# Optimization experiments

Hardware: AMD Instinct MI355X
Metric: run time of the kernel (lower is better)

The kernel has to match this reference:

```python
import jax, jax.numpy as jnp
import numpy as np

NL, NQ, FD, HD, NH = 6, 128, 256, 512, 8
NC, B, T, H, W = 6, 1, 1, 48, 120
PPF = 24 // 6  # points_per_face
P = PPF * PPF * 6  # code emits (num_points//6)^2 points per face = 96 total
NPARAM, NTYPE, NATTR = 11, 10, 3
PMIN = np.array([-50., -50., -5., -15., -15., -5., -5., -3.14, 0.5, 0.5, 0.5], np.float32)
PMAX = np.array([50., 50., 5., 15., 15., 5., 5., 3.14, 10., 5., 3.], np.float32)


def _box_template():
    off = np.linspace(-0.4, 0.4, PPF).astype(np.float32)
    pts = []
    for axis in range(3):  # -x,+x,-y,+y,-z,+z faces, same order as torch code
        for s in (-0.5, 0.5):
            rem = [a for a in range(3) if a != axis]
            for i in range(PPF):
                for j in range(PPF):
                    p = [0.0, 0.0, 0.0]
                    p[axis] = s
                    p[rem[0]] = off[i]
                    p[rem[1]] = off[j]
                    pts.append(p)
    return np.asarray(pts, np.float32)  # [P,3]

TPL = _box_template()


def _mlp2(x, w1, b1, w2, b2):
    return jax.nn.relu(x @ w1.T + b1) @ w2.T + b2


def _ln(x, g, b):
    m = x.mean(-1, keepdims=True)
    v = ((x - m) ** 2).mean(-1, keepdims=True)
    return (x - m) * jax.lax.rsqrt(v + 1e-5) * g + b


def _mha(q, k, v, in_w, in_b, out_w, out_b):
    hd = HD // NH
    wq, wk, wv = jnp.split(in_w, 3, axis=0)
    bq, bk, bv = jnp.split(in_b, 3)
    def heads(x, w, b):
        y = x @ w.T + b
        return y.reshape(x.shape[0], x.shape[1], NH, hd).transpose(0, 2, 1, 3)
    Q, K, V = heads(q, wq, bq), heads(k, wk, bk), heads(v, wv, bv)
    a = jax.nn.softmax(jnp.einsum('bhqd,bhkd->bhqk', Q, K) * (hd ** -0.5), axis=-1)
    o = jnp.einsum('bhqk,bhkd->bhqd', a, V)
    o = o.transpose(0, 2, 1, 3).reshape(q.shape[0], q.shape[1], HD)
    return o @ out_w.T + out_b


def _sample_box_points(motion):
    # motion [B,N,11] -> [B,N,P,3]; indices: X0 Y1 Z2 .. YAW7 L8 W9 H10
    c = motion[..., 0:3]
    dims = motion[..., 8:11]
    yaw = motion[..., 7]
    p = TPL * dims[:, :, None, :]  # [B,N,P,3]
    cy, sy = jnp.cos(yaw)[..., None], jnp.sin(yaw)[..., None]
    xr = p[..., 0] * cy - p[..., 1] * sy
    yr = p[..., 0] * sy + p[..., 1] * cy
    return jnp.stack([xr, yr, p[..., 2]], -1) + c[:, :, None, :]


def _gather_aggregate(pts, features, proj):
    # pts [B,N,P,3]; features [NC,B,T,C,H,W]; proj [NC,3,4]
    Bb, N, Pp, _ = pts.shape
    NP = N * Pp
    hom = jnp.concatenate([pts, jnp.ones_like(pts[..., :1])], -1)
    feat_flat = features.reshape(NC, Bb, T, FD, H * W)
    acc = jnp.zeros((Bb, FD, NP), features.dtype)
    for cidx in range(NC):
        cam = jnp.einsum('ij,bnpj->bnpi', proj[cidx], hom)  # [B,N,P,3]
        z = cam[..., 2]
        zs = jnp.where(jnp.abs(z) > 1e-6, z, 1e-6)
        u = (cam[..., 0] / zs).reshape(Bb, NP)
        v = (cam[..., 1] / zs).reshape(Bb, NP)
        front = (z > 0).reshape(Bb, NP)
        u0, v0 = jnp.floor(u), jnp.floor(v)
        du, dv = u - u0, v - v0
        cam_acc = jnp.zeros((Bb, T, FD, NP), features.dtype)
        for (ui, vi, wgt) in ((u0, v0, (1 - du) * (1 - dv)),
                              (u0 + 1, v0, du * (1 - dv)),
                              (u0, v0 + 1, (1 - du) * dv),
                              (u0 + 1, v0 + 1, du * dv)):
            ok = front & (ui >= 0) & (ui <= W - 1) & (vi >= 0) & (vi <= H - 1)
            idx = (jnp.clip(vi, 0, H - 1) * W + jnp.clip(ui, 0, W - 1)).astype(jnp.int32)
            bidx = jnp.broadcast_to(idx[:, None, None, :], (Bb, T, FD, NP))
            g = jnp.take_along_axis(feat_flat[cidx], bidx, axis=-1)
            cam_acc = cam_acc + g * (wgt * ok)[:, None, None, :]
        acc = acc + cam_acc.mean(axis=1)  # mean over time
    agg = (acc / NC).reshape(Bb, FD, N, Pp).mean(-1)  # mean over cams and points
    return agg.transpose(0, 2, 1)  # [B,N,C]

_ga = jax.checkpoint(_gather_aggregate)


def _forward(features, proj, ego_states, queries0, param_min, param_max, motion_w1, motion_b1, motion_w2, motion_b2, type_w1, type_b1, type_w2, type_b2, attr_w1, attr_b1, attr_w2, attr_b2, fmlp_w1, fmlp_b1, fmlp_w2, fmlp_b2, sa_in_w, sa_in_b, sa_out_w, sa_out_b, fa_in_w, fa_in_b, fa_out_w, fa_out_b, ffn_w1, ffn_b1, ffn_w2, ffn_b2, ln1_g, ln1_b, ln2_g, ln2_b, ln3_g, ln3_b):
    Bb = features.shape[1]
    q = jnp.broadcast_to(queries0, (Bb, NQ, HD))
    preds = []
    for i in range(NL):
        motion = jax.nn.sigmoid(_mlp2(q, motion_w1, motion_b1, motion_w2, motion_b2)) * (param_max - param_min) + param_min
        tlog = _mlp2(q, type_w1, type_b1, type_w2, type_b2)
        attr = jax.nn.sigmoid(_mlp2(q, attr_w1, attr_b1, attr_w2, attr_b2))
        preds.append(jnp.concatenate([motion, tlog, attr], -1))
        if i == NL - 1:
            break  # last layer only predicts (layers[-1] unused, as in torch code)
        pts = _sample_box_points(motion)
        agg = _ga(pts, features, proj)
        feat_h = _mlp2(agg, fmlp_w1, fmlp_b1, fmlp_w2, fmlp_b2)
        x = _ln(q, ln1_g[i], ln1_b[i])
        x = x + _mha(x, x, x, sa_in_w[i], sa_in_b[i], sa_out_w[i], sa_out_b[i])
        x = _ln(x, ln2_g[i], ln2_b[i])
        x = x + _mha(x, feat_h, feat_h, fa_in_w[i], fa_in_b[i], fa_out_w[i], fa_out_b[i])
        x = _ln(x, ln3_g[i], ln3_b[i])
        q = x + _mlp2(x, ffn_w1[i], ffn_b1[i], ffn_w2[i], ffn_b2[i])
    return jnp.stack(preds)  # [NL,B,NQ,24]


def setup_inputs() -> dict:
    key = jax.random.key(0)
    ks = iter(jax.random.split(key, 64))
    def g(shape, s=0.02):
        return jax.random.normal(next(ks), shape, jnp.float32) * s
    fx, cx, cy = 40.0, W / 2.0, H / 2.0
    Ps = []
    for c in range(NC):
        th = 2.0 * np.pi * c / NC
        Rm = np.stack([np.array([-np.sin(th), np.cos(th), 0.0]),
                       np.array([0.0, 0.0, -1.0]),
                       np.array([np.cos(th), np.sin(th), 0.0])])
        K = np.array([[fx, 0.0, cx], [0.0, fx, cy], [0.0, 0.0, 1.0]])
        Pm = np.zeros((3, 4))
        Pm[:, :3] = K @ Rm
        Ps.append(Pm)
    inp = dict(
        features=jax.random.normal(next(ks), (NC, B, T, FD, H, W), jnp.float32),
        proj=jnp.asarray(np.asarray(Ps, np.float32)),
        ego_states=jax.random.normal(next(ks), (B, T, 5), jnp.float32),
        queries0=g((1, NQ, HD), 1.0),
        param_min=jnp.asarray(PMIN), param_max=jnp.asarray(PMAX),
        motion_w1=g((HD, HD)), motion_b1=jnp.zeros((HD,)),
        motion_w2=g((NPARAM, HD)), motion_b2=jnp.zeros((NPARAM,)),
        type_w1=g((HD, HD)), type_b1=jnp.zeros((HD,)),
        type_w2=g((NTYPE, HD)), type_b2=jnp.zeros((NTYPE,)),
        attr_w1=g((HD, HD)), attr_b1=jnp.zeros((HD,)),
        attr_w2=g((NATTR, HD)), attr_b2=jnp.zeros((NATTR,)),
        fmlp_w1=g((HD, FD)), fmlp_b1=jnp.zeros((HD,)),
        fmlp_w2=g((HD, HD)), fmlp_b2=jnp.zeros((HD,)),
        sa_in_w=g((NL, 3 * HD, HD)), sa_in_b=jnp.zeros((NL, 3 * HD)),
        sa_out_w=g((NL, HD, HD)), sa_out_b=jnp.zeros((NL, HD)),
        fa_in_w=g((NL, 3 * HD, HD)), fa_in_b=jnp.zeros((NL, 3 * HD)),
        fa_out_w=g((NL, HD, HD)), fa_out_b=jnp.zeros((NL, HD)),
        ffn_w1=g((NL, 4 * HD, HD)), ffn_b1=jnp.zeros((NL, 4 * HD)),
        ffn_w2=g((NL, HD, 4 * HD)), ffn_b2=jnp.zeros((NL, HD)),
        ln1_g=jnp.ones((NL, HD)), ln1_b=jnp.zeros((NL, HD)),
        ln2_g=jnp.ones((NL, HD)), ln2_b=jnp.zeros((NL, HD)),
        ln3_g=jnp.ones((NL, HD)), ln3_b=jnp.zeros((NL, HD)),
    )
    return inp


def reference(features, proj, ego_states, queries0, param_min, param_max, motion_w1, motion_b1, motion_w2, motion_b2, type_w1, type_b1, type_w2, type_b2, attr_w1, attr_b1, attr_w2, attr_b2, fmlp_w1, fmlp_b1, fmlp_w2, fmlp_b2, sa_in_w, sa_in_b, sa_out_w, sa_out_b, fa_in_w, fa_in_b, fa_out_w, fa_out_b, ffn_w1, ffn_b1, ffn_w2, ffn_b2, ln1_g, ln1_b, ln2_g, ln2_b, ln3_g, ln3_b):
    return _forward(features, proj, ego_states, queries0, param_min, param_max, motion_w1, motion_b1, motion_w2, motion_b2, type_w1, type_b1, type_w2, type_b2, attr_w1, attr_b1, attr_w2, attr_b2, fmlp_w1, fmlp_b1, fmlp_w2, fmlp_b2, sa_in_w, sa_in_b, sa_out_w, sa_out_b, fa_in_w, fa_in_b, fa_out_w, fa_out_b, ffn_w1, ffn_b1, ffn_w2, ffn_b2, ln1_g, ln1_b, ln2_g, ln2_b, ln3_g, ln3_b)
```

## Files before the change

### kernel.cpp

```cpp
#include <hip/hip_runtime.h>
#include <hip/hip_bf16.h>

typedef __hip_bfloat16 bf16;
typedef _Float16 h16;
typedef __attribute__((ext_vector_type(8))) _Float16 half8;
typedef __attribute__((ext_vector_type(4))) _Float16 half4;
typedef __attribute__((ext_vector_type(4))) float f32x4;

#define NQ 128
#define HD 512
#define FD 256
#define NC 6
#define IMH 48
#define IMW 120
#define HW 5760

__device__ __forceinline__ half8 pack8(float4 x, float4 y) {
    half8 h;
    h[0] = (h16)x.x; h[1] = (h16)x.y; h[2] = (h16)x.z; h[3] = (h16)x.w;
    h[4] = (h16)y.x; h[5] = (h16)y.y; h[6] = (h16)y.z; h[7] = (h16)y.w;
    return h;
}

__global__ __launch_bounds__(256) void transpose_feat_k(const float* __restrict__ f,
                                                        bf16* __restrict__ ft)
{
    __shared__ float tile[32][33];
    int cam = blockIdx.z;
    int hw0 = blockIdx.x * 32, fd0 = blockIdx.y * 32;
    int tx = threadIdx.x, ty = threadIdx.y;
    const float* fb = f + (size_t)cam * FD * HW;
    for (int r = ty; r < 32; r += 8)
        tile[r][tx] = fb[(size_t)(fd0 + r) * HW + hw0 + tx];
    __syncthreads();
    bf16* fo = ft + (size_t)cam * HW * FD;
    for (int r = ty; r < 32; r += 8)
        fo[(size_t)(hw0 + r) * FD + fd0 + tx] = __float2bfloat16(tile[tx][r]);
}

__global__ __launch_bounds__(256) void cvt16_k(const float* __restrict__ src,
                                               h16* __restrict__ dst, int n)
{
    int i = blockIdx.x * 256 + threadIdx.x;
    if (i < n) dst[i] = (h16)src[i];
}

struct SwzDesc {
    const float* src[11];
    unsigned int chunkStart[12];
    unsigned int tileStart[11];
    int K[11];
};

__device__ __forceinline__ int lperm(int lane, int ksl) {
    return lane ^ ((lane >> 4) & 3) ^ (ksl << 2);
}

__global__ __launch_bounds__(256) void swizzle3_k(SwzDesc d, h16* __restrict__ dst)
{
    __shared__ h16 fbuf[4096];
    int bid = blockIdx.x;
    int w = 0;
    while (bid >= (int)d.chunkStart[w + 1]) w++;
    int local = bid - (int)d.chunkStart[w];
    int Kk = d.K[w];
    int kc = Kk >> 6;
    int n64 = local / kc, kchunk = local - n64 * kc;
    int t = threadIdx.x;

    int rr  = t >> 4;
    int cb  = (t & 15) * 4;
    int ksl = (t >> 3) & 1;
    int kk  = cb & 31;
    int laneb = ((kk >> 3) << 4) + rr;
    int elemB = (kk & 7) * 2;
    const float* sbase = d.src[w] + (size_t)(n64 * 64 + rr) * Kk + kchunk * 64 + cb;
#pragma unroll
    for (int rp = 0; rp < 4; rp++) {
        float4 u = *(const float4*)(sbase + (size_t)rp * 16 * Kk);
        int tile8 = ksl * 4 + rp;
        int l2 = lperm(laneb, ksl);
        half4* fp = (half4*)((char*)fbuf + tile8 * 1024 + l2 * 16 + elemB);
        half4 hv; hv[0] = (h16)u.x; hv[1] = (h16)u.y; hv[2] = (h16)u.z; hv[3] = (h16)u.w;
        *fp = hv;
    }
    __syncthreads();

    int K32 = Kk >> 5;
#pragma unroll
    for (int i = 0; i < 2; i++) {
        int hidx = t + i * 256;
        int tl = hidx >> 6, within = hidx & 63;
        int ksl2 = tl >> 2, ctt = tl & 3;
        int l2 = lperm(within, ksl2);
        size_t tileg = (size_t)d.tileStart[w]
                     + ((size_t)n64 * K32 + (kchunk * 2 + ksl2)) * 4 + ctt;
        *(half8*)(dst + tileg * 512 + within * 8) =
            *(const half8*)((const char*)fbuf + tl * 1024 + l2 * 16);
    }
}

template<int CTN, int NSUM, bool A2SW, bool LNA>
__global__ __launch_bounds__(256) void gemm_sk4(
    const h16* __restrict__ A16, int lda, int sumStride,
    const float* __restrict__ A32,
    const float* __restrict__ lng, const float* __restrict__ lnb,
    float* __restrict__ lnout,
    const h16* __restrict__ A2_16, int a2Start,
    const h16* __restrict__ Wswz,
    const float* __restrict__ B0, const float* __restrict__ B1, const float* __restrict__ B2s,
    const float* __restrict__ R, int ldr,
    float* __restrict__ C32, h16* __restrict__ C16, int ldc,
    int K, int act)
{
    __shared__ float redu[CTN * 4 * 256];
    __shared__ float sst[64], sst2[64];
    int bx = blockIdx.x, by = blockIdx.y;
    int tid = threadIdx.x;
    int w = tid >> 6, l = tid & 63;
    int lr = l & 15, q4 = l >> 4;
    int m0 = by * 16;
    int n0 = bx * 16 * CTN;
    int row = m0 + lr;
    int K32 = K >> 5;
    int KQ = K32 >> 2;
    int ks0 = w * KQ;

    bool useA2 = A2SW && (bx >= a2Start);

    const float* arow32 = nullptr;
    float mean = 0.f, rstd = 1.f;
    if (LNA && !useA2) {
        arow32 = A32 + (size_t)row * K + q4 * 8;
        float s = 0.f, s2 = 0.f;
        for (int ks = ks0; ks < ks0 + KQ; ks++) {
            float4 u = *(const float4*)(arow32 + ks * 32);
            float4 v = *(const float4*)(arow32 + ks * 32 + 4);
            s  += u.x + u.y + u.z + u.w + v.x + v.y + v.z + v.w;
            s2 += u.x*u.x + u.y*u.y + u.z*u.z + u.w*u.w
                + v.x*v.x + v.y*v.y + v.z*v.z + v.w*v.w;
        }
        s  += __shfl_xor(s, 16);  s  += __shfl_xor(s, 32);
        s2 += __shfl_xor(s2, 16); s2 += __shfl_xor(s2, 32);
        if (q4 == 0) { sst[w * 16 + lr] = s; sst2[w * 16 + lr] = s2; }
        __syncthreads();
        float st = sst[lr] + sst[16 + lr] + sst[32 + lr] + sst[48 + lr];
        float st2 = sst2[lr] + sst2[16 + lr] + sst2[32 + lr] + sst2[48 + lr];
        mean = st * (1.0f / (float)K);
        float var = st2 * (1.0f / (float)K) - mean * mean;
        rstd = rsqrtf(var + 1e-5f);
    }

    const h16* arow16 = nullptr;
    if (useA2)       arow16 = A2_16 + (size_t)row * 512 + q4 * 8;
    else if (!LNA)   arow16 = A16 + (size_t)row * lda + q4 * 8;

    const h16* wbase[CTN];
#pragma unroll
    for (int ct = 0; ct < CTN; ct++) {
        int tct = (n0 >> 4) + ct;
        wbase[ct] = Wswz + (((size_t)(tct >> 2) * K32 * 4 + (tct & 3)) * 64 + l) * 8;
    }

    f32x4 acc[CTN];
#pragma unroll
    for (int ct = 0; ct < CTN; ct++) acc[ct] = (f32x4){0.f, 0.f, 0.f, 0.f};

    bool wrln = LNA && !useA2 && (bx == 0) && lnout;

#pragma unroll 4
    for (int ks = ks0; ks < ks0 + KQ; ks++) {
        half8 a;
        if (LNA && !useA2) {
            float4 u = *(const float4*)(arow32 + ks * 32);
            float4 v = *(const float4*)(arow32 + ks * 32 + 4);
            float4 g0 = *(const float4*)(lng + ks * 32 + q4 * 8);
            float4 g1 = *(const float4*)(lng + ks * 32 + q4 * 8 + 4);
            float4 b0 = *(const float4*)(lnb + ks * 32 + q4 * 8);
            float4 b1 = *(const float4*)(lnb + ks * 32 + q4 * 8 + 4);
            float4 o0, o1;
            o0.x = (u.x - mean) * rstd * g0.x + b0.x;
            o0.y = (u.y - mean) * rstd * g0.y + b0.y;
            o0.z = (u.z - mean) * rstd * g0.z + b0.z;
            o0.w = (u.w - mean) * rstd * g0.w + b0.w;
            o1.x = (v.x - mean) * rstd * g1.x + b1.x;
            o1.y = (v.y - mean) * rstd * g1.y + b1.y;
            o1.z = (v.z - mean) * rstd * g1.z + b1.z;
            o1.w = (v.w - mean) * rstd * g1.w + b1.w;
            if (wrln) {
                *(float4*)(lnout + (size_t)row * K + ks * 32 + q4 * 8)     = o0;
                *(float4*)(lnout + (size_t)row * K + ks * 32 + q4 * 8 + 4) = o1;
            }
            a = pack8(o0, o1);
        } else if (NSUM == 1) {
            a = *(const half8*)(arow16 + (size_t)ks * 32);
        } else {
            float s[8] = {0.f, 0.f, 0.f, 0.f, 0.f, 0.f, 0.f, 0.f};
#pragma unroll
            for (int j = 0; j < NSUM; j++) {
                half8 tt = *(const half8*)(arow16 + (size_t)j * sumStride + ks * 32);
#pragma unroll
                for (int e = 0; e < 8; e++) s[e] += (float)tt[e];
            }
#pragma unroll
            for (int e = 0; e < 8; e++) a[e] = (h16)s[e];
        }
#pragma unroll
        for (int ct = 0; ct < CTN; ct++) {
            half8 bfr = *(const half8*)(wbase[ct] + (size_t)ks * 2048);
            acc[ct] = __builtin_amdgcn_mfma_f32_16x16x32_f16(a, bfr, acc[ct], 0, 0, 0);
        }
    }

#pragma unroll
    for (int ct = 0; ct < CTN; ct++)
        *(f32x4*)&redu[(size_t)(w * CTN + ct) * 256 + l * 4] = acc[ct];
    __syncthreads();

    if (w < CTN) {
        int ct = w;
        f32x4 sum = *(const f32x4*)&redu[(size_t)ct * 256 + l * 4];
#pragma unroll
        for (int w2 = 1; w2 < 4; w2++) {
            f32x4 tt = *(const f32x4*)&redu[(size_t)(w2 * CTN + ct) * 256 + l * 4];
            sum[0] += tt[0]; sum[1] += tt[1]; sum[2] += tt[2]; sum[3] += tt[3];
        }
        int n = n0 + ct * 16 + lr;
        float bv;
        if (B1) { int sec = n >> 9, ni = n & 511;
                  bv = (sec == 0) ? B0[ni] : (sec == 1 ? B1[ni] : B2s[ni]); }
        else bv = B0[n];
#pragma unroll
        for (int r = 0; r < 4; r++) {
            int m = m0 + q4 * 4 + r;
            float v = sum[r] + bv;
            if (act) v = fmaxf(v, 0.f);
            if (R) v += R[(size_t)m * ldr + n];
            if (C32) C32[(size_t)m * ldc + n] = v;
            if (C16) C16[(size_t)m * ldc + n] = (h16)v;
        }
    }
}

__global__ __launch_bounds__(64) void heads2_k(const h16* __restrict__ hid16,
                                               const float* __restrict__ w2m, const float* __restrict__ b2m,
                                               const float* __restrict__ w2t, const float* __restrict__ b2t,
                                               const float* __restrict__ w2a, const float* __restrict__ b2a,
                                               const float* __restrict__ pmin, const float* __restrict__ pmax,
                                               float* __restrict__ out)
{
    int q = blockIdx.x, n = blockIdx.y, lane = threadIdx.x;
    const float* wr; float bv; int mode, sect;
    if (n < 11)      { sect = 0; wr = w2m + n * 512;        bv = b2m[n];      mode = 0; }
    else if (n < 21) { sect = 1; wr = w2t + (n - 11) * 512; bv = b2t[n - 11]; mode = 1; }
    else             { sect = 2; wr = w2a + (n - 21) * 512; bv = b2a[n - 21]; mode = 2; }
    half8 hv = *(const half8*)(hid16 + q * 1536 + sect * 512 + lane * 8);
    const float4* w4 = (const float4*)(wr + lane * 8);
    float4 c0 = w4[0], c1 = w4[1];
    float acc = (float)hv[0] * c0.x + (float)hv[1] * c0.y
              + (float)hv[2] * c0.z + (float)hv[3] * c0.w
              + (float)hv[4] * c1.x + (float)hv[5] * c1.y
              + (float)hv[6] * c1.z + (float)hv[7] * c1.w;
    for (int off = 32; off; off >>= 1) acc += __shfl_xor(acc, off);
    if (lane == 0) {
        float v = acc + bv;
        if (mode == 0)      v = (1.0f / (1.0f + __expf(-v))) * (pmax[n] - pmin[n]) + pmin[n];
        else if (mode == 2) v = 1.0f / (1.0f + __expf(-v));
        out[q * 24 + n] = v;
    }
}

__global__ __launch_bounds__(256) void attn_k(const float* __restrict__ qkv,
                                              h16* __restrict__ out16)
{
    __shared__ float KVl[128 * 68];
    __shared__ float Ql[32 * 68];
    __shared__ float Pl[32 * 128];
    int h = blockIdx.x >> 2, chunk = blockIdx.x & 3;
    int tid = threadIdx.x;

    for (int l = tid; l < 2048; l += 256) {
        int row = l >> 4, c4 = (l & 15) * 4;
        float4 v = *(const float4*)&qkv[row * 1536 + 512 + h * 64 + c4];
        *(float4*)&KVl[row * 68 + c4] = v;
    }
    for (int l = tid; l < 512; l += 256) {
        int row = l >> 4, c4 = (l & 15) * 4;
        float4 v = *(const float4*)&qkv[(chunk * 32 + row) * 1536 + h * 64 + c4];
        *(float4*)&Ql[row * 68 + c4] = v;
    }
    __syncthreads();

    int w = tid >> 6, j = tid & 63;
    for (int r8 = 0; r8 < 8; r8++) {
        int lr = w * 8 + r8;
        float s0 = 0.f, s1 = 0.f;
#pragma unroll
        for (int k4 = 0; k4 < 64; k4 += 4) {
            float4 qv  = *(const float4*)&Ql[lr * 68 + k4];
            float4 k0v = *(const float4*)&KVl[j * 68 + k4];
            float4 k1v = *(const float4*)&KVl[(j + 64) * 68 + k4];
            s0 += qv.x * k0v.x + qv.y * k0v.y + qv.z * k0v.z + qv.w * k0v.w;
            s1 += qv.x * k1v.x + qv.y * k1v.y + qv.z * k1v.z + qv.w * k1v.w;
        }
        s0 *= 0.125f; s1 *= 0.125f;
        float m = fmaxf(s0, s1);
        for (int off = 32; off; off >>= 1) m = fmaxf(m, __shfl_xor(m, off));
        float e0 = __expf(s0 - m), e1 = __expf(s1 - m);
        float sm = e0 + e1;
        for (int off = 32; off; off >>= 1) sm += __shfl_xor(sm, off);
        float inv = 1.0f / sm;
        Pl[lr * 128 + j]      = e0 * inv;
        Pl[lr * 128 + j + 64] = e1 * inv;
    }
    __syncthreads();

    for (int l = tid; l < 2048; l += 256) {
        int row = l >> 4, c4 = (l & 15) * 4;
        float4 v = *(const float4*)&qkv[row * 1536 + 1024 + h * 64 + c4];
        KVl[(c4 + 0) * 132 + row] = v.x;
        KVl[(c4 + 1) * 132 + row] = v.y;
        KVl[(c4 + 2) * 132 + row] = v.z;
        KVl[(c4 + 3) * 132 + row] = v.w;
    }
    __syncthreads();

    int d = tid & 63, w2 = tid >> 6;
    for (int r8 = 0; r8 < 8; r8++) {
        int lr = w2 * 8 + r8;
        float o = 0.f;
#pragma unroll
        for (int j4 = 0; j4 < 128; j4 += 4) {
            float4 pv = *(const float4*)&Pl[lr * 128 + j4];
            float4 vv = *(const float4*)&KVl[d * 132 + j4];
            o += pv.x * vv.x + pv.y * vv.y + pv.z * vv.z + pv.w * vv.w;
        }
        out16[(chunk * 32 + lr) * 512 + h * 64 + d] = (h16)o;
    }
}

__device__ __forceinline__ float bflo(unsigned u) {
    union { unsigned i; float f; } c; c.i = u << 16; return c.f;
}
__device__ __forceinline__ float bfhi(unsigned u) {
    union { unsigned i; float f; } c; c.i = u & 0xffff0000u; return c.f;
}

__global__ __launch_bounds__(256) void gather_k(const bf16* __restrict__ ft,
                                                const float* __restrict__ proj,
                                                const float* __restrict__ preds,
                                                h16* __restrict__ agg16)
{
    __shared__ float mo[11];
    __shared__ int   goff[384];
    __shared__ float gw[384];
    __shared__ int   cnt;
    __shared__ float part[8][256];
    int n = blockIdx.x, cam = blockIdx.y, tid = threadIdx.x;
    if (tid == 0) cnt = 0;
    if (tid < 11) mo[tid] = preds[n * 24 + tid];
    __syncthreads();

    if (tid < 96) {
        int p = tid;
        float dd0 = mo[8], dd1 = mo[9], dd2 = mo[10];
        float c0 = mo[0], c1 = mo[1], c2 = mo[2];
        float sy, cy;
        sincosf(mo[7], &sy, &cy);
        int face = p >> 4, axis = face >> 1;
        float sgn = (face & 1) ? 0.5f : -0.5f;
        float offi = -0.4f + (float)((p >> 2) & 3) * (0.8f / 3.0f);
        float offj = -0.4f + (float)(p & 3) * (0.8f / 3.0f);
        float t0, t1, t2;
        if (axis == 0)      { t0 = sgn;  t1 = offi; t2 = offj; }
        else if (axis == 1) { t0 = offi; t1 = sgn;  t2 = offj; }
        else                { t0 = offi; t1 = offj; t2 = sgn;  }
        float px = t0 * dd0, py = t1 * dd1, pz = t2 * dd2;
        float X = px * cy - py * sy + c0;
        float Y = px * sy + py * cy + c1;
        float Z = pz + c2;
        const float* P = proj + cam * 12;
        float cu = P[0] * X + P[1] * Y + P[2] * Z + P[3];
        float cv = P[4] * X + P[5] * Y + P[6] * Z + P[7];
        float cz = P[8] * X + P[9] * Y + P[10] * Z + P[11];
        float zs = (fabsf(cz) > 1e-6f) ? cz : 1e-6f;
        float u = cu / zs, v = cv / zs;
        bool front = cz > 0.0f;
        float u0 = floorf(u), v0 = floorf(v);
        float du = u - u0, dv = v - v0;
        float us[4] = {u0, u0 + 1.0f, u0, u0 + 1.0f};
        float vs[4] = {v0, v0, v0 + 1.0f, v0 + 1.0f};
        float wt[4] = {(1.0f - du) * (1.0f - dv), du * (1.0f - dv),
                       (1.0f - du) * dv, du * dv};
        int   myoff[4]; float myw[4]; int k = 0;
#pragma unroll
        for (int t = 0; t < 4; t++) {
            bool ok = front && (us[t] >= 0.0f) && (us[t] <= 119.0f)
                            && (vs[t] >= 0.0f) && (vs[t] <= 47.0f)
                            && (wt[t] > 0.0f);
            if (ok) {
                myoff[k] = ((int)vs[t] * IMW + (int)us[t]) * FD;
                myw[k]   = wt[t];
                k++;
            }
        }
        if (k) {
            int base = atomicAdd(&cnt, k);
            for (int s = 0; s < k; s++) { goff[base + s] = myoff[s]; gw[base + s] = myw[s]; }
        }
    }
    __syncthreads();
    int C = cnt;
    h16* slab = agg16 + (size_t)cam * 32768 + n * 256;
    if (C == 0) { slab[tid] = (h16)0.f; return; }

    int g8  = (tid & 31) * 8;
    int row = tid >> 5;
    const bf16* fb = ft + (size_t)cam * HW * FD + g8;
    float acc[8] = {0.f, 0.f, 0.f, 0.f, 0.f, 0.f, 0.f, 0.f};
    for (int e = row; e < C; e += 8) {
        float w = gw[e];
        uint4 rv = *(const uint4*)(fb + goff[e]);
        acc[0] += w * bflo(rv.x); acc[1] += w * bfhi(rv.x);
        acc[2] += w * bflo(rv.y); acc[3] += w * bfhi(rv.y);
        acc[4] += w * bflo(rv.z); acc[5] += w * bfhi(rv.z);
        acc[6] += w * bflo(rv.w); acc[7] += w * bfhi(rv.w);
    }
#pragma unroll
    for (int j = 0; j < 8; j++) part[row][g8 + j] = acc[j];
    __syncthreads();
    float s = 0.f;
#pragma unroll
    for (int r = 0; r < 8; r++) s += part[r][tid];
    slab[tid] = (h16)(s * (1.0f / 576.0f));
}

extern "C" void kernel_launch(void* const* d_in, const int* in_sizes, int n_in,
                              void* d_out, int out_size, void* d_ws, size_t ws_size,
                              hipStream_t stream)
{
    const float* features  = (const float*)d_in[0];
    const float* proj      = (const float*)d_in[1];
    const float* queries0  = (const float*)d_in[3];
    const float* pmin      = (const float*)d_in[4];
    const float* pmax      = (const float*)d_in[5];
    const float* motion_w1 = (const float*)d_in[6];
    const float* motion_b1 = (const float*)d_in[7];
    const float* motion_w2 = (const float*)d_in[8];
    const float* motion_b2 = (const float*)d_in[9];
    const float* type_w1   = (const float*)d_in[10];
    const float* type_b1   = (const float*)d_in[11];
    const float* type_w2   = (const float*)d_in[12];
    const float* type_b2   = (const float*)d_in[13];
    const float* attr_w1   = (const float*)d_in[14];
    const float* attr_b1   = (const float*)d_in[15];
    const float* attr_w2   = (const float*)d_in[16];
    const float* attr_b2   = (const float*)d_in[17];
    const float* fmlp_w1   = (const float*)d_in[18];
    const float* fmlp_b1   = (const float*)d_in[19];
    const float* fmlp_w2   = (const float*)d_in[20];
    const float* fmlp_b2   = (const float*)d_in[21];
    const float* sa_in_w   = (const float*)d_in[22];
    const float* sa_in_b   = (const float*)d_in[23];
    const float* sa_out_w  = (const float*)d_in[24];
    const float* sa_out_b  = (const float*)d_in[25];
    const float* fa_in_w   = (const float*)d_in[26];
    const float* fa_in_b   = (const float*)d_in[27];
    const float* fa_out_w  = (const float*)d_in[28];
    const float* fa_out_b  = (const float*)d_in[29];
    const float* ffn_w1    = (const float*)d_in[30];
    const float* ffn_b1    = (const float*)d_in[31];
    const float* ffn_w2    = (const float*)d_in[32];
    const float* ffn_b2    = (const float*)d_in[33];
    const float* ln1_g     = (const float*)d_in[34];
    const float* ln1_b     = (const float*)d_in[35];
    const float* ln2_g     = (const float*)d_in[36];
    const float* ln2_b     = (const float*)d_in[37];
    const float* ln3_g     = (const float*)d_in[38];
    const float* ln3_b     = (const float*)d_in[39];
    float* out = (float*)d_out;

    char* p = (char*)d_ws;
    bf16* feat_t = (bf16*)p;   p += (size_t)NC * HW * FD * 2;
    h16* swz     = (h16*)p;    p += (size_t)51456 * 512 * 2;
    h16* q016    = (h16*)p;    p += 65536 * 2;
    h16* hid16   = (h16*)p;    p += 196608 * 2;
    h16* agg16   = (h16*)p;    p += 196608 * 2;
    h16* fmlph16 = (h16*)p;    p += 65536 * 2;
    h16* feath16 = (h16*)p;    p += 65536 * 2;
    h16* attnb16 = (h16*)p;    p += 65536 * 2;
    h16* ffnh16  = (h16*)p;    p += 262144 * 2;
    h16* qn16    = (h16*)p;    p += 65536 * 2;
    float* qkv   = (float*)p;  p += 196608 * 4;
    float* lnx   = (float*)p;  p += 65536 * 4;
    float* x1    = (float*)p;  p += 65536 * 4;
    float* x2    = (float*)p;  p += 65536 * 4;
    float* qn32  = (float*)p;  p += 65536 * 4;

    SwzDesc sd;
    const float* srcs[11] = {motion_w1, type_w1, attr_w1, fmlp_w1, fmlp_w2,
                             sa_in_w, sa_out_w, fa_in_w, fa_out_w, ffn_w1, ffn_w2};
    int Ks[11]    = {512, 512, 512, 256, 512, 512, 512, 512, 512, 512, 2048};
    int tiles[11] = {512, 512, 512, 256, 512, 9216, 3072, 9216, 3072, 12288, 12288};
    unsigned int cumT = 0, cumC = 0;
    for (int i = 0; i < 11; i++) {
        sd.src[i] = srcs[i]; sd.K[i] = Ks[i];
        sd.tileStart[i] = cumT; sd.chunkStart[i] = cumC;
        cumT += tiles[i]; cumC += tiles[i] >> 3;
    }
    sd.chunkStart[11] = cumC;

    swizzle3_k<<<6432, 256, 0, stream>>>(sd, swz);
    cvt16_k<<<256, 256, 0, stream>>>(queries0, q016, 65536);
    transpose_feat_k<<<dim3(180, 8, 6), dim3(32, 8), 0, stream>>>(features, feat_t);

    const h16* sw_heads = swz;
    const h16* sw_fmlp1 = swz + 786432;
    const h16* sw_fmlp2 = swz + 917504;
    const h16* sw_sain  = swz + 1179648;
    const h16* sw_saout = swz + 5898240;
    const h16* sw_fain  = swz + 7471104;
    const h16* sw_faout = swz + 12189696;
    const h16* sw_ffn1  = swz + 13762560;
    const h16* sw_ffn2  = swz + 20054016;

    const h16*   q16 = q016;
    const float* q32 = queries0;

    for (int i = 0; i < 6; i++) {
        gemm_sk4<2, 1, false, false><<<dim3(48, 8), 256, 0, stream>>>(
            q16, 512, 0, nullptr, nullptr, nullptr, nullptr, nullptr, 0,
            sw_heads, motion_b1, type_b1, attr_b1, nullptr, 0,
            nullptr, hid16, 1536, 512, 1);
        heads2_k<<<dim3(128, 24), 64, 0, stream>>>(hid16, motion_w2, motion_b2,
                                                   type_w2, type_b2, attr_w2, attr_b2,
                                                   pmin, pmax, out + i * 3072);
        if (i == 5) break;

        gather_k<<<dim3(128, 6), 256, 0, stream>>>(feat_t, proj, out + i * 3072, agg16);
        gemm_sk4<1, 6, false, false><<<dim3(32, 8), 256, 0, stream>>>(
            agg16, 256, 32768, nullptr, nullptr, nullptr, nullptr, nullptr, 0,
            sw_fmlp1, fmlp_b1, nullptr, nullptr, nullptr, 0,
            nullptr, fmlph16, 512, 256, 1);
        gemm_sk4<1, 1, false, false><<<dim3(32, 8), 256, 0, stream>>>(
            fmlph16, 512, 0, nullptr, nullptr, nullptr, nullptr, nullptr, 0,
            sw_fmlp2, fmlp_b2, nullptr, nullptr, nullptr, 0,
            nullptr, feath16, 512, 512, 0);

        gemm_sk4<2, 1, false, true><<<dim3(48, 8), 256, 0, stream>>>(
            nullptr, 0, 0, q32, ln1_g + i * 512, ln1_b + i * 512, lnx, nullptr, 0,
            sw_sain + (size_t)i * 786432, sa_in_b + i * 1536, nullptr, nullptr,
            nullptr, 0, qkv, nullptr, 1536, 512, 0);
        attn_k<<<32, 256, 0, stream>>>(qkv, attnb16);
        gemm_sk4<1, 1, false, false><<<dim3(32, 8), 256, 0, stream>>>(
            attnb16, 512, 0, nullptr, nullptr, nullptr, nullptr, nullptr, 0,
            sw_saout + (size_t)i * 262144, sa_out_b + i * 512, nullptr, nullptr,
            lnx, 512, x1, nullptr, 512, 512, 0);

        gemm_sk4<2, 1, true, true><<<dim3(48, 8), 256, 0, stream>>>(
            nullptr, 0, 0, x1, ln2_g + i * 512, ln2_b + i * 512, lnx, feath16, 16,
            sw_fain + (size_t)i * 786432, fa_in_b + i * 1536, nullptr, nullptr,
            nullptr, 0, qkv, nullptr, 1536, 512, 0);
        attn_k<<<32, 256, 0, stream>>>(qkv, attnb16);
        gemm_sk4<1, 1, false, false><<<dim3(32, 8), 256, 0, stream>>>(
            attnb16, 512, 0, nullptr, nullptr, nullptr, nullptr, nullptr, 0,
            sw_faout + (size_t)i * 262144, fa_out_b + i * 512, nullptr, nullptr,
            lnx, 512, x2, nullptr, 512, 512, 0);

        gemm_sk4<2, 1, false, true><<<dim3(64, 8), 256, 0, stream>>>(
            nullptr, 0, 0, x2, ln3_g + i * 512, ln3_b + i * 512, lnx, nullptr, 0,
            sw_ffn1 + (size_t)i * 1048576, ffn_b1 + i * 2048, nullptr, nullptr,
            nullptr, 0, nullptr, ffnh16, 2048, 512, 1);
        gemm_sk4<1, 1, false, false><<<dim3(32, 8), 256, 0, stream>>>(
            ffnh16, 2048, 0, nullptr, nullptr, nullptr, nullptr, nullptr, 0,
            sw_ffn2 + (size_t)i * 1048576, ffn_b2 + i * 512, nullptr, nullptr,
            lnx, 512, qn32, qn16, 512, 2048, 0);

        q16 = qn16;
        q32 = qn32;
    }
}
```

Measured before the change: 863.5 us.

## Merge independent kernels into horizontally fused launches to cut launch count

The three setup kernels (weight swizzle, feature transpose, query conversion) become one prep kernel that dispatches on block index. Inside the decoder loop, independent pieces of work now share a launch: heads2 with the self-attention input projection, fmlp1 with self-attention, and fmlp2 with the self-attention output projection. This reorders the stage schedule to reduce kernel launch overhead and fill the GPU with more concurrent blocks. The cost is larger shared memory per block in the fused kernels and heterogeneous blocks, which can lower occupancy.

```diff
diff --git a/kernel.cpp b/kernel.cpp
--- a/kernel.cpp
+++ b/kernel.cpp
@@ -22,27 +22,20 @@
     return h;
 }
 
-__global__ __launch_bounds__(256) void transpose_feat_k(const float* __restrict__ f,
-                                                        bf16* __restrict__ ft)
-{
-    __shared__ float tile[32][33];
-    int cam = blockIdx.z;
-    int hw0 = blockIdx.x * 32, fd0 = blockIdx.y * 32;
-    int tx = threadIdx.x, ty = threadIdx.y;
+
+__device__ __forceinline__ void transpose_body(int bx, int by, int cam,
+                                               int tx, int ty, float* tile,
+                                               const float* __restrict__ f,
+                                               bf16* __restrict__ ft)
+{
+    int hw0 = bx * 32, fd0 = by * 32;
     const float* fb = f + (size_t)cam * FD * HW;
     for (int r = ty; r < 32; r += 8)
-        tile[r][tx] = fb[(size_t)(fd0 + r) * HW + hw0 + tx];
+        tile[r * 33 + tx] = fb[(size_t)(fd0 + r) * HW + hw0 + tx];
     __syncthreads();
     bf16* fo = ft + (size_t)cam * HW * FD;
     for (int r = ty; r < 32; r += 8)
-        fo[(size_t)(hw0 + r) * FD + fd0 + tx] = __float2bfloat16(tile[tx][r]);
-}
-
-__global__ __launch_bounds__(256) void cvt16_k(const float* __restrict__ src,
-                                               h16* __restrict__ dst, int n)
-{
-    int i = blockIdx.x * 256 + threadIdx.x;
-    if (i < n) dst[i] = (h16)src[i];
+        fo[(size_t)(hw0 + r) * FD + fd0 + tx] = __float2bfloat16(tile[tx * 33 + r]);
 }
 
 struct SwzDesc {
@@ -56,17 +49,15 @@
     return lane ^ ((lane >> 4) & 3) ^ (ksl << 2);
 }
 
-__global__ __launch_bounds__(256) void swizzle3_k(SwzDesc d, h16* __restrict__ dst)
-{
-    __shared__ h16 fbuf[4096];
-    int bid = blockIdx.x;
+__device__ __forceinline__ void swizzle_body(int bid, int t, h16* fbuf,
+                                             const SwzDesc& d, h16* __restrict__ dst)
+{
     int w = 0;
     while (bid >= (int)d.chunkStart[w + 1]) w++;
     int local = bid - (int)d.chunkStart[w];
     int Kk = d.K[w];
     int kc = Kk >> 6;
     int n64 = local / kc, kchunk = local - n64 * kc;
-    int t = threadIdx.x;
 
     int rr  = t >> 4;
     int cb  = (t & 15) * 4;
@@ -101,7 +92,8 @@
 }
 
 template<int CTN, int NSUM, bool A2SW, bool LNA>
-__global__ __launch_bounds__(256) void gemm_sk4(
+__device__ __forceinline__ void gemm_body(int bx, int by, int tid,
+    float* redu, float* sst, float* sst2,
     const h16* __restrict__ A16, int lda, int sumStride,
     const float* __restrict__ A32,
     const float* __restrict__ lng, const float* __restrict__ lnb,
@@ -113,10 +105,6 @@
     float* __restrict__ C32, h16* __restrict__ C16, int ldc,
     int K, int act)
 {
-    __shared__ float redu[CTN * 4 * 256];
-    __shared__ float sst[64], sst2[64];
-    int bx = blockIdx.x, by = blockIdx.y;
-    int tid = threadIdx.x;
     int w = tid >> 6, l = tid & 63;
     int lr = l & 15, q4 = l >> 4;
     int m0 = by * 16;
@@ -242,14 +230,14 @@
     }
 }
 
-__global__ __launch_bounds__(64) void heads2_k(const h16* __restrict__ hid16,
-                                               const float* __restrict__ w2m, const float* __restrict__ b2m,
-                                               const float* __restrict__ w2t, const float* __restrict__ b2t,
-                                               const float* __restrict__ w2a, const float* __restrict__ b2a,
-                                               const float* __restrict__ pmin, const float* __restrict__ pmax,
-                                               float* __restrict__ out)
-{
-    int q = blockIdx.x, n = blockIdx.y, lane = threadIdx.x;
+__device__ __forceinline__ void heads2_body(int q, int n, int lane,
+    const h16* __restrict__ hid16,
+    const float* __restrict__ w2m, const float* __restrict__ b2m,
+    const float* __restrict__ w2t, const float* __restrict__ b2t,
+    const float* __restrict__ w2a, const float* __restrict__ b2a,
+    const float* __restrict__ pmin, const float* __restrict__ pmax,
+    float* __restrict__ out)
+{
     const float* wr; float bv; int mode, sect;
     if (n < 11)      { sect = 0; wr = w2m + n * 512;        bv = b2m[n];      mode = 0; }
     else if (n < 21) { sect = 1; wr = w2t + (n - 11) * 512; bv = b2t[n - 11]; mode = 1; }
@@ -270,14 +258,12 @@
     }
 }
 
-__global__ __launch_bounds__(256) void attn_k(const float* __restrict__ qkv,
-                                              h16* __restrict__ out16)
-{
-    __shared__ float KVl[128 * 68];
-    __shared__ float Ql[32 * 68];
-    __shared__ float Pl[32 * 128];
-    int h = blockIdx.x >> 2, chunk = blockIdx.x & 3;
-    int tid = threadIdx.x;
+__device__ __forceinline__ void attn_body(int bid, int tid,
+                                          float* KVl, float* Ql, float* Pl,
+                                          const float* __restrict__ qkv,
+                                          h16* __restrict__ out16)
+{
+    int h = bid >> 2, chunk = bid & 3;
 
     for (int l = tid; l < 2048; l += 256) {
         int row = l >> 4, c4 = (l & 15) * 4;
@@ -336,6 +322,135 @@
             o += pv.x * vv.x + pv.y * vv.y + pv.z * vv.z + pv.w * vv.w;
         }
         out16[(chunk * 32 + lr) * 512 + h * 64 + d] = (h16)o;
+    }
+}
+
+
+__global__ __launch_bounds__(256) void prep_k(SwzDesc d, h16* __restrict__ swz,
+                                              const float* __restrict__ feat,
+                                              bf16* __restrict__ feat_t,
+                                              const float* __restrict__ q0,
+                                              h16* __restrict__ q016)
+{
+    __shared__ char shm[8448];
+    int bid = blockIdx.x, t = threadIdx.x;
+    if (bid < 6432) {
+        swizzle_body(bid, t, (h16*)shm, d, swz);
+    } else if (bid < 15072) {
+        int tb = bid - 6432;
+        transpose_body(tb % 180, (tb / 180) % 8, tb / 1440, t & 31, t >> 5,
+                       (float*)shm, feat, feat_t);
+    } else {
+        int i = (bid - 15072) * 256 + t;
+        q016[i] = (h16)q0[i];
+    }
+}
+
+template<int CTN, int NSUM, bool A2SW, bool LNA>
+__global__ __launch_bounds__(256) void gemm_sk4(
+    const h16* __restrict__ A16, int lda, int sumStride,
+    const float* __restrict__ A32,
+    const float* __restrict__ lng, const float* __restrict__ lnb,
+    float* __restrict__ lnout,
+    const h16* __restrict__ A2_16, int a2Start,
+    const h16* __restrict__ Wswz,
+    const float* __restrict__ B0, const float* __restrict__ B1, const float* __restrict__ B2s,
+    const float* __restrict__ R, int ldr,
+    float* __restrict__ C32, h16* __restrict__ C16, int ldc,
+    int K, int act)
+{
+    __shared__ float redu[CTN * 4 * 256];
+    __shared__ float sst[64], sst2[64];
+    gemm_body<CTN, NSUM, A2SW, LNA>(blockIdx.x, blockIdx.y, threadIdx.x,
+        redu, sst, sst2, A16, lda, sumStride, A32, lng, lnb, lnout, A2_16, a2Start,
+        Wswz, B0, B1, B2s, R, ldr, C32, C16, ldc, K, act);
+}
+
+__global__ __launch_bounds__(64) void heads2_k(const h16* __restrict__ hid16,
+                                               const float* __restrict__ w2m, const float* __restrict__ b2m,
+                                               const float* __restrict__ w2t, const float* __restrict__ b2t,
+                                               const float* __restrict__ w2a, const float* __restrict__ b2a,
+                                               const float* __restrict__ pmin, const float* __restrict__ pmax,
+                                               float* __restrict__ out)
+{
+    heads2_body(blockIdx.x, blockIdx.y, threadIdx.x,
+                hid16, w2m, b2m, w2t, b2t, w2a, b2a, pmin, pmax, out);
+}
+
+__global__ __launch_bounds__(256) void attn_k(const float* __restrict__ qkv,
+                                              h16* __restrict__ out16)
+{
+    __shared__ float KVl[128 * 68];
+    __shared__ float Ql[32 * 68];
+    __shared__ float Pl[32 * 128];
+    attn_body(blockIdx.x, threadIdx.x, KVl, Ql, Pl, qkv, out16);
+}
+
+__global__ __launch_bounds__(256) void d2_k(
+    const float* __restrict__ q32, const float* __restrict__ lng,
+    const float* __restrict__ lnb, float* __restrict__ lnx,
+    const h16* __restrict__ Wsain, const float* __restrict__ Bsain,
+    float* __restrict__ qkv,
+    const h16* __restrict__ hid16,
+    const float* __restrict__ w2m, const float* __restrict__ b2m,
+    const float* __restrict__ w2t, const float* __restrict__ b2t,
+    const float* __restrict__ w2a, const float* __restrict__ b2a,
+    const float* __restrict__ pmin, const float* __restrict__ pmax,
+    float* __restrict__ out)
+{
+    __shared__ float redu[2 * 4 * 256];
+    __shared__ float sst[64], sst2[64];
+    int x = blockIdx.x, by = blockIdx.y, tid = threadIdx.x;
+    if (x < 48) {
+        gemm_body<2, 1, false, true>(x, by, tid, redu, sst, sst2,
+            nullptr, 0, 0, q32, lng, lnb, lnx, nullptr, 0,
+            Wsain, Bsain, nullptr, nullptr, nullptr, 0,
+            qkv, nullptr, 1536, 512, 0);
+    } else {
+        int p = (((x - 48) * 8 + by) << 2) + (tid >> 6);
+        heads2_body(p / 24, p % 24, tid & 63,
+                    hid16, w2m, b2m, w2t, b2t, w2a, b2a, pmin, pmax, out);
+    }
+}
+
+__global__ __launch_bounds__(256) void d4_k(
+    const h16* __restrict__ agg16, const h16* __restrict__ Wf1,
+    const float* __restrict__ Bf1, h16* __restrict__ fmlph16,
+    const float* __restrict__ qkv, h16* __restrict__ attnb16)
+{
+    __shared__ float smem[14976];
+    int x = blockIdx.x, by = blockIdx.y, tid = threadIdx.x;
+    if (x < 32) {
+        gemm_body<1, 6, false, false>(x, by, tid, smem, smem + 1024, smem + 1088,
+            agg16, 256, 32768, nullptr, nullptr, nullptr, nullptr, nullptr, 0,
+            Wf1, Bf1, nullptr, nullptr, nullptr, 0,
+            nullptr, fmlph16, 512, 256, 1);
+    } else {
+        int slot = (x - 32) * 8 + by;
+        attn_body(slot, tid, smem, smem + 8704, smem + 10880, qkv, attnb16);
+    }
+}
+
+__global__ __launch_bounds__(256) void d5_k(
+    const h16* __restrict__ fmlph16, const h16* __restrict__ Wf2,
+    const float* __restrict__ Bf2, h16* __restrict__ feath16,
+    const h16* __restrict__ attnb16, const h16* __restrict__ Wso,
+    const float* __restrict__ Bso, const float* __restrict__ lnx,
+    float* __restrict__ x1)
+{
+    __shared__ float redu[1024];
+    __shared__ float sst[64], sst2[64];
+    int x = blockIdx.x, by = blockIdx.y, tid = threadIdx.x;
+    if (x < 32) {
+        gemm_body<1, 1, false, false>(x, by, tid, redu, sst, sst2,
+            fmlph16, 512, 0, nullptr, nullptr, nullptr, nullptr, nullptr, 0,
+            Wf2, Bf2, nullptr, nullptr, nullptr, 0,
+            nullptr, feath16, 512, 512, 0);
+    } else {
+        gemm_body<1, 1, false, false>(x - 32, by, tid, redu, sst, sst2,
+            attnb16, 512, 0, nullptr, nullptr, nullptr, nullptr, nullptr, 0,
+            Wso, Bso, nullptr, nullptr, lnx, 512,
+            x1, nullptr, 512, 512, 0);
     }
 }
 
@@ -510,9 +625,7 @@
     }
     sd.chunkStart[11] = cumC;
 
-    swizzle3_k<<<6432, 256, 0, stream>>>(sd, swz);
-    cvt16_k<<<256, 256, 0, stream>>>(queries0, q016, 65536);
-    transpose_feat_k<<<dim3(180, 8, 6), dim3(32, 8), 0, stream>>>(features, feat_t);
+    prep_k<<<15328, 256, 0, stream>>>(sd, swz, features, feat_t, queries0, q016);
 
     const h16* sw_heads = swz;
     const h16* sw_fmlp1 = swz + 786432;
@@ -532,36 +645,36 @@
             q16, 512, 0, nullptr, nullptr, nullptr, nullptr, nullptr, 0,
             sw_heads, motion_b1, type_b1, attr_b1, nullptr, 0,
             nullptr, hid16, 1536, 512, 1);
-        heads2_k<<<dim3(128, 24), 64, 0, stream>>>(hid16, motion_w2, motion_b2,
-                                                   type_w2, type_b2, attr_w2, attr_b2,
-                                                   pmin, pmax, out + i * 3072);
-        if (i == 5) break;
+
+        if (i == 5) {
+            heads2_k<<<dim3(128, 24), 64, 0, stream>>>(hid16, motion_w2, motion_b2,
+                                                       type_w2, type_b2, attr_w2, attr_b2,
+                                                       pmin, pmax, out + i * 3072);
+            break;
+        }
+
+        d2_k<<<dim3(144, 8), 256, 0, stream>>>(
+            q32, ln1_g + i * 512, ln1_b + i * 512, lnx,
+            sw_sain + (size_t)i * 786432, sa_in_b + i * 1536, qkv,
+            hid16, motion_w2, motion_b2, type_w2, type_b2, attr_w2, attr_b2,
+            pmin, pmax, out + i * 3072);
 
         gather_k<<<dim3(128, 6), 256, 0, stream>>>(feat_t, proj, out + i * 3072, agg16);
-        gemm_sk4<1, 6, false, false><<<dim3(32, 8), 256, 0, stream>>>(
-            agg16, 256, 32768, nullptr, nullptr, nullptr, nullptr, nullptr, 0,
-            sw_fmlp1, fmlp_b1, nullptr, nullptr, nullptr, 0,
-            nullptr, fmlph16, 512, 256, 1);
-        gemm_sk4<1, 1, false, false><<<dim3(32, 8), 256, 0, stream>>>(
-            fmlph16, 512, 0, nullptr, nullptr, nullptr, nullptr, nullptr, 0,
-            sw_fmlp2, fmlp_b2, nullptr, nullptr, nullptr, 0,
-            nullptr, feath16, 512, 512, 0);
-
-        gemm_sk4<2, 1, false, true><<<dim3(48, 8), 256, 0, stream>>>(
-            nullptr, 0, 0, q32, ln1_g + i * 512, ln1_b + i * 512, lnx, nullptr, 0,
-            sw_sain + (size_t)i * 786432, sa_in_b + i * 1536, nullptr, nullptr,
-            nullptr, 0, qkv, nullptr, 1536, 512, 0);
-        attn_k<<<32, 256, 0, stream>>>(qkv, attnb16);
-        gemm_sk4<1, 1, false, false><<<dim3(32, 8), 256, 0, stream>>>(
-            attnb16, 512, 0, nullptr, nullptr, nullptr, nullptr, nullptr, 0,
-            sw_saout + (size_t)i * 262144, sa_out_b + i * 512, nullptr, nullptr,
-            lnx, 512, x1, nullptr, 512, 512, 0);
+
+        d4_k<<<dim3(36, 8), 256, 0, stream>>>(
+            agg16, sw_fmlp1, fmlp_b1, fmlph16, qkv, attnb16);
+
+        d5_k<<<dim3(64, 8), 256, 0, stream>>>(
+            fmlph16, sw_fmlp2, fmlp_b2, feath16,
+            attnb16, sw_saout + (size_t)i * 262144, sa_out_b + i * 512, lnx, x1);
 
         gemm_sk4<2, 1, true, true><<<dim3(48, 8), 256, 0, stream>>>(
             nullptr, 0, 0, x1, ln2_g + i * 512, ln2_b + i * 512, lnx, feath16, 16,
             sw_fain + (size_t)i * 786432, fa_in_b + i * 1536, nullptr, nullptr,
             nullptr, 0, qkv, nullptr, 1536, 512, 0);
+
         attn_k<<<32, 256, 0, stream>>>(qkv, attnb16);
+
         gemm_sk4<1, 1, false, false><<<dim3(32, 8), 256, 0, stream>>>(
             attnb16, 512, 0, nullptr, nullptr, nullptr, nullptr, nullptr, 0,
             sw_faout + (size_t)i * 262144, fa_out_b + i * 512, nullptr, nullptr,
@@ -571,6 +684,7 @@
             nullptr, 0, 0, x2, ln3_g + i * 512, ln3_b + i * 512, lnx, nullptr, 0,
             sw_ffn1 + (size_t)i * 1048576, ffn_b1 + i * 2048, nullptr, nullptr,
             nullptr, 0, nullptr, ffnh16, 2048, 512, 1);
+
         gemm_sk4<1, 1, false, false><<<dim3(32, 8), 256, 0, stream>>>(
             ffnh16, 2048, 0, nullptr, nullptr, nullptr, nullptr, nullptr, 0,
             sw_ffn2 + (size_t)i * 1048576, ffn_b2 + i * 512, nullptr, nullptr,
```

Result: faster. 815.1 us (-5.6%).
